# Kernel tuning notes

Measured on AMD Instinct MI355X. Metric: run time of the kernel, lower is better.

The kernel has to match this reference:

```python
import jax, jax.numpy as jnp
import numpy as np

# SamplesLoss(loss='sinkhorn', p=1, blur=0.05): entropic regularization eps = blur**p = 0.05,
# debiased Sinkhorn divergence S(a,b) = OT(a,b) - 0.5*OT(a,a) - 0.5*OT(b,b).
EPS = 0.05
N_ITER = 50
N_POINTS = 32


def _cost(X, Y):
    # p=1 cost: Euclidean distance. X:[B,N,D] Y:[B,M,D] -> [B,N,M]
    d2 = jnp.sum((X[:, :, None, :] - Y[:, None, :, :]) ** 2, axis=-1)
    return jnp.sqrt(d2 + 1e-12)


def _ot(X, Y):
    # log-domain Sinkhorn with uniform weights; returns dual cost <mu,f>+<nu,g> per batch.
    B, N, _ = X.shape
    M = Y.shape[1]
    C = _cost(X, Y)  # [B,N,M]
    log_mu = jnp.full((B, N), -np.log(N), C.dtype)
    log_nu = jnp.full((B, M), -np.log(M), C.dtype)

    def body(carry, _):
        f, g = carry
        f = -EPS * jax.nn.logsumexp((g[:, None, :] - C) / EPS + log_nu[:, None, :], axis=2)
        g = -EPS * jax.nn.logsumexp((f[:, :, None] - C) / EPS + log_mu[:, :, None], axis=1)
        return (f, g), None

    init = (jnp.zeros((B, N), C.dtype), jnp.zeros((B, M), C.dtype))
    (f, g), _ = jax.lax.scan(body, init, None, length=N_ITER)
    return jnp.mean(f, axis=-1) + jnp.mean(g, axis=-1)  # uniform weights => mean


def _sinkhorn_div(X, Y):
    return _ot(X, Y) - 0.5 * _ot(X, X) - 0.5 * _ot(Y, Y)


def _encode(x, W, edge_index):
    # simple 1-layer GCN-style encoder: linear + mean neighbor aggregation + self, ReLU
    h = x @ W  # [n_nodes, emb_dim]
    src, dst = edge_index[0], edge_index[1]
    n = x.shape[0]
    agg = jax.ops.segment_sum(h[src], dst, num_segments=n)
    deg = jax.ops.segment_sum(jnp.ones(src.shape, h.dtype), dst, num_segments=n)
    return jax.nn.relu(h + agg / jnp.maximum(deg, 1.0)[:, None])


def setup_inputs() -> dict:
    key = jax.random.key(0)
    k1, k2, k3, k4, k5 = jax.random.split(key, 5)
    n_nodes, d_feat, emb_dim = 50000, 128, 256
    n_edges, n_pairs = 800000, 8192
    x = jax.random.normal(k1, (n_nodes, d_feat), jnp.float32)
    W = jax.random.normal(k2, (d_feat, emb_dim), jnp.float32) / np.sqrt(d_feat)
    edge_index = jax.random.randint(k3, (2, n_edges), 0, n_nodes, jnp.int64)
    pairs = jax.random.randint(k4, (2, n_pairs), 0, n_nodes, jnp.int64)
    graph_dist = jax.random.uniform(k5, (n_pairs,), jnp.float32, 1.0, 5.0)
    return {"x": x, "W": W, "edge_index": edge_index, "pairs": pairs,
            "graph_dist": graph_dist}


def reference(x, W, edge_index, pairs, graph_dist):
    z = _encode(x, W, edge_index)                       # [n_nodes, emb_dim]
    B = pairs.shape[1]
    Xa = z[pairs[0]].reshape(B, N_POINTS, -1)           # [B, n_points, space_dim]
    Xb = z[pairs[1]].reshape(B, N_POINTS, -1)
    distance = _sinkhorn_div(Xa, Xb)                    # = -score_pairs
    distortion = jnp.abs(distance - graph_dist) / graph_dist
    return jnp.mean(distortion)
```

## Files before the change

kernel.cpp:

```cpp
#include <hip/hip_runtime.h>

#define N_NODES 50000
#define N_EDGES 800000
#define N_PAIRS 8192
#define N_SLOTS (2 * N_PAIRS)
#define CAP     64

#define INV_EPS   20.0f
#define LOG2E_F   1.4426950408889634f
#define LN2_F     0.6931471805599453f
#define LN32_F    3.4657359027997265f
#define EPS_F     0.05f

typedef float f2 __attribute__((ext_vector_type(2)));

__global__ void k_mark(const int* __restrict__ pairs, int* __restrict__ flags) {
    int t = blockIdx.x * 256 + threadIdx.x;
    if (t < N_SLOTS) flags[pairs[t]] = 1;
}

__global__ __launch_bounds__(256) void k_scatter(
        const int* __restrict__ eidx, const int* __restrict__ flags,
        int* __restrict__ cnt, int* __restrict__ bucket) {
    int t = blockIdx.x * 256 + threadIdx.x;
    int dst = eidx[N_EDGES + t];
    if (!flags[dst]) return;
    int pos = atomicAdd(&cnt[dst], 1);
    if (pos < CAP) bucket[dst * CAP + pos] = eidx[t];
}

__global__ __launch_bounds__(256) void k_gemm(
        const int* __restrict__ pairs, const float* __restrict__ x,
        const int* __restrict__ cnt, const int* __restrict__ bucket,
        const float* __restrict__ W, float* __restrict__ Z) {
    __shared__ __align__(16) float Us[16 * 128];
    int sbase = blockIdx.x * 16;
    int t = threadIdx.x;
    int wave = t >> 6, lane = t & 63;

    #pragma unroll
    for (int rr = 0; rr < 4; ++rr) {
        int r = wave * 4 + rr;
        int node = pairs[sbase + r];
        int n = cnt[node];
        int m = (n < CAP) ? n : CAP;
        const int* bk = bucket + node * CAP;
        float ax = 0.0f, ay = 0.0f;
        int k = 0;
        for (; k + 4 <= m; k += 4) {
            int s0 = bk[k], s1 = bk[k + 1], s2 = bk[k + 2], s3 = bk[k + 3];
            float2 v0 = *(const float2*)(x + (size_t)s0 * 128 + lane * 2);
            float2 v1 = *(const float2*)(x + (size_t)s1 * 128 + lane * 2);
            float2 v2 = *(const float2*)(x + (size_t)s2 * 128 + lane * 2);
            float2 v3 = *(const float2*)(x + (size_t)s3 * 128 + lane * 2);
            ax += (v0.x + v1.x) + (v2.x + v3.x);
            ay += (v0.y + v1.y) + (v2.y + v3.y);
        }
        for (; k < m; ++k) {
            int s0 = bk[k];
            float2 v0 = *(const float2*)(x + (size_t)s0 * 128 + lane * 2);
            ax += v0.x;
            ay += v0.y;
        }
        float rdeg = 1.0f / fmaxf((float)n, 1.0f);
        float2 xv = *(const float2*)(x + (size_t)node * 128 + lane * 2);
        float2 o;
        o.x = fmaf(ax, rdeg, xv.x);
        o.y = fmaf(ay, rdeg, xv.y);
        *(float2*)(Us + r * 128 + lane * 2) = o;
    }
    __syncthreads();

    int jq = t & 63;
    int rq = t >> 6;
    float acc[4][4] = {};
    const float4* Wv = (const float4*)W;

    for (int k4 = 0; k4 < 32; ++k4) {
        float4 wv[4];
        #pragma unroll
        for (int i = 0; i < 4; ++i) wv[i] = Wv[(size_t)(k4 * 4 + i) * 64 + jq];
        #pragma unroll
        for (int r = 0; r < 4; ++r) {
            float4 uv = *(const float4*)(Us + (rq * 4 + r) * 128 + k4 * 4);
            float uk0 = uv.x, uk1 = uv.y, uk2 = uv.z, uk3 = uv.w;
            acc[r][0] = fmaf(uk0, wv[0].x, acc[r][0]);
            acc[r][1] = fmaf(uk0, wv[0].y, acc[r][1]);
            acc[r][2] = fmaf(uk0, wv[0].z, acc[r][2]);
            acc[r][3] = fmaf(uk0, wv[0].w, acc[r][3]);
            acc[r][0] = fmaf(uk1, wv[1].x, acc[r][0]);
            acc[r][1] = fmaf(uk1, wv[1].y, acc[r][1]);
            acc[r][2] = fmaf(uk1, wv[1].z, acc[r][2]);
            acc[r][3] = fmaf(uk1, wv[1].w, acc[r][3]);
            acc[r][0] = fmaf(uk2, wv[2].x, acc[r][0]);
            acc[r][1] = fmaf(uk2, wv[2].y, acc[r][1]);
            acc[r][2] = fmaf(uk2, wv[2].z, acc[r][2]);
            acc[r][3] = fmaf(uk2, wv[2].w, acc[r][3]);
            acc[r][0] = fmaf(uk3, wv[3].x, acc[r][0]);
            acc[r][1] = fmaf(uk3, wv[3].y, acc[r][1]);
            acc[r][2] = fmaf(uk3, wv[3].z, acc[r][2]);
            acc[r][3] = fmaf(uk3, wv[3].w, acc[r][3]);
        }
    }

    #pragma unroll
    for (int r = 0; r < 4; ++r) {
        float4 o;
        o.x = fmaxf(acc[r][0], 0.0f);
        o.y = fmaxf(acc[r][1], 0.0f);
        o.z = fmaxf(acc[r][2], 0.0f);
        o.w = fmaxf(acc[r][3], 0.0f);
        *(float4*)(Z + (size_t)(sbase + rq * 4 + r) * 256 + jq * 4) = o;
    }
}

__global__ __launch_bounds__(128) void k_sinkhorn(
        const float* __restrict__ Z, float* __restrict__ dist) {
    __shared__ __align__(16) float smem[2][1280];

    int w = threadIdx.x >> 6;
    int lane = threadIdx.x & 63;
    float* S = &smem[w][0];
    const float CSCALE = -INV_EPS * LOG2E_F;
    const float CBIAS  = -LN32_F * LOG2E_F;

    if (blockIdx.x < 2048) {
        int h = lane >> 5, i = lane & 31;
        int q = (i >> 4) & 1;
        int ip = i ^ 16;
        int P0 = blockIdx.x * 4 + w * 2;

        float* sP   = S;
        float* swv0 = S + 512;
        float* spv0 = S + 576;
        float* swv1 = S + 640;
        float* spv1 = S + 704;

        f2 KA0[8], KB0[8], KA1[8], KB1[8];

        auto build = [&](f2 (&KA)[8], f2 (&KB)[8], int P) {
            int src = h ? (N_PAIRS + P) : P;
            float* sPh = sP + h * 256;
            {
                const float4* zp = (const float4*)(Z + (size_t)src * 256);
                *(float4*)(&sPh[i * 8])     = zp[i * 2];
                *(float4*)(&sPh[i * 8 + 4]) = zp[i * 2 + 1];
            }
            const f2* xp = (const f2*)(&sPh[i * 8]);
            f2 x0 = xp[0], x1 = xp[1], x2 = xp[2], x3 = xp[3];
            const f2* bp = (const f2*)(&sPh[ip * 8]);
            f2 b0 = bp[0], b1 = bp[1], b2 = bp[2], b3 = bp[3];
            #pragma unroll
            for (int t = 0; t < 16; ++t) {
                int j = q * 16 + t;
                const f2* yp = (const f2*)(&sPh[j * 8]);
                f2 y0 = yp[0], y1 = yp[1], y2 = yp[2], y3 = yp[3];
                f2 d, s2;
                d = x0 - y0; s2 = d * d;
                d = x1 - y1; s2 = __builtin_elementwise_fma(d, d, s2);
                d = x2 - y2; s2 = __builtin_elementwise_fma(d, d, s2);
                d = x3 - y3; s2 = __builtin_elementwise_fma(d, d, s2);
                float d2 = s2.x + s2.y + 1e-12f;
                KA[t >> 1][t & 1] = __builtin_amdgcn_exp2f(
                    fmaf(__builtin_amdgcn_sqrtf(d2), CSCALE, CBIAS));
                d = b0 - y0; s2 = d * d;
                d = b1 - y1; s2 = __builtin_elementwise_fma(d, d, s2);
                d = b2 - y2; s2 = __builtin_elementwise_fma(d, d, s2);
                d = b3 - y3; s2 = __builtin_elementwise_fma(d, d, s2);
                float e2 = s2.x + s2.y + 1e-12f;
                KB[t >> 1][t & 1] = __builtin_amdgcn_exp2f(
                    fmaf(__builtin_amdgcn_sqrtf(e2), CSCALE, CBIAS));
            }
        };
        build(KA0, KB0, P0);
        build(KA1, KB1, P0 + 1);

        float pp0 = 0.0f, pp1 = 0.0f, E0 = 1.0f, E1 = 1.0f;
        float w0c = 1.0f, w0p = 1.0f, w1c = 1.0f, w1p = 1.0f;
        swv0[lane] = 1.0f;
        swv1[lane] = 1.0f;

        const int blens[9] = {4, 12, 12, 12, 12, 12, 12, 12, 12};
        #pragma unroll 1
        for (int blk = 0; blk < 9; ++blk) {
            int L = blens[blk];
            #pragma unroll 1
            for (int s = 0; s < L; ++s) {
                const float4* wp0 = (const float4*)(&swv0[h * 32 + q * 16]);
                const float4* wp1 = (const float4*)(&swv1[h * 32 + q * 16]);
                float4 A0 = wp0[0], A1 = wp0[1], A2 = wp0[2], A3 = wp0[3];
                float4 B0 = wp1[0], B1 = wp1[1], B2 = wp1[2], B3 = wp1[3];
                f2 aA0 = KA0[0] * f2{A0.x, A0.y};
                f2 aA1 = KA0[1] * f2{A0.z, A0.w};
                f2 aB0 = KB0[0] * f2{A0.x, A0.y};
                f2 aB1 = KB0[1] * f2{A0.z, A0.w};
                aA0 = __builtin_elementwise_fma(KA0[2], f2{A1.x, A1.y}, aA0);
                aA1 = __builtin_elementwise_fma(KA0[3], f2{A1.z, A1.w}, aA1);
                aB0 = __builtin_elementwise_fma(KB0[2], f2{A1.x, A1.y}, aB0);
                aB1 = __builtin_elementwise_fma(KB0[3], f2{A1.z, A1.w}, aB1);
                aA0 = __builtin_elementwise_fma(KA0[4], f2{A2.x, A2.y}, aA0);
                aA1 = __builtin_elementwise_fma(KA0[5], f2{A2.z, A2.w}, aA1);
                aB0 = __builtin_elementwise_fma(KB0[4], f2{A2.x, A2.y}, aB0);
                aB1 = __builtin_elementwise_fma(KB0[5], f2{A2.z, A2.w}, aB1);
                aA0 = __builtin_elementwise_fma(KA0[6], f2{A3.x, A3.y}, aA0);
                aA1 = __builtin_elementwise_fma(KA0[7], f2{A3.z, A3.w}, aA1);
                aB0 = __builtin_elementwise_fma(KB0[6], f2{A3.x, A3.y}, aB0);
                aB1 = __builtin_elementwise_fma(KB0[7], f2{A3.z, A3.w}, aB1);
                f2 aa0 = aA0 + aA1;
                f2 bb0 = aB0 + aB1;
                float pa0 = aa0.x + aa0.y;
                float pb0 = bb0.x + bb0.y;
                f2 cA0 = KA1[0] * f2{B0.x, B0.y};
                f2 cA1 = KA1[1] * f2{B0.z, B0.w};
                f2 cB0 = KB1[0] * f2{B0.x, B0.y};
                f2 cB1 = KB1[1] * f2{B0.z, B0.w};
                cA0 = __builtin_elementwise_fma(KA1[2], f2{B1.x, B1.y}, cA0);
                cA1 = __builtin_elementwise_fma(KA1[3], f2{B1.z, B1.w}, cA1);
                cB0 = __builtin_elementwise_fma(KB1[2], f2{B1.x, B1.y}, cB0);
                cB1 = __builtin_elementwise_fma(KB1[3], f2{B1.z, B1.w}, cB1);
                cA0 = __builtin_elementwise_fma(KA1[4], f2{B2.x, B2.y}, cA0);
                cA1 = __builtin_elementwise_fma(KA1[5], f2{B2.z, B2.w}, cA1);
                cB0 = __builtin_elementwise_fma(KB1[4], f2{B2.x, B2.y}, cB0);
                cB1 = __builtin_elementwise_fma(KB1[5], f2{B2.z, B2.w}, cB1);
                cA0 = __builtin_elementwise_fma(KA1[6], f2{B3.x, B3.y}, cA0);
                cA1 = __builtin_elementwise_fma(KA1[7], f2{B3.z, B3.w}, cA1);
                cB0 = __builtin_elementwise_fma(KB1[6], f2{B3.x, B3.y}, cB0);
                cB1 = __builtin_elementwise_fma(KB1[7], f2{B3.z, B3.w}, cB1);
                f2 aa1 = cA0 + cA1;
                f2 bb1 = cB0 + cB1;
                float pa1 = aa1.x + aa1.y;
                float pb1 = bb1.x + bb1.y;
                float o0 = __shfl_xor(pb0, 16);
                float o1 = __shfl_xor(pb1, 16);
                w0p = w0c;
                w0c = __builtin_amdgcn_rcpf(pa0 + o0) * E0;
                w1p = w1c;
                w1c = __builtin_amdgcn_rcpf(pa1 + o1) * E1;
                swv0[h * 32 + i] = w0c;
                swv1[h * 32 + i] = w1c;
            }
            if (blk < 8) {
                float d0 = __builtin_amdgcn_logf(w0c);
                float d1 = __builtin_amdgcn_logf(w1c);
                pp0 += d0;
                pp1 += d1;
                spv0[h * 32 + i] = d0;
                spv1[h * 32 + i] = d1;
                {
                    const float4* dv = (const float4*)(&spv0[h * 32 + q * 16]);
                    float4 D0 = dv[0], D1 = dv[1], D2 = dv[2], D3 = dv[3];
                    float ex[16];
                    ex[0]  = __builtin_amdgcn_exp2f(D0.x);
                    ex[1]  = __builtin_amdgcn_exp2f(D0.y);
                    ex[2]  = __builtin_amdgcn_exp2f(D0.z);
                    ex[3]  = __builtin_amdgcn_exp2f(D0.w);
                    ex[4]  = __builtin_amdgcn_exp2f(D1.x);
                    ex[5]  = __builtin_amdgcn_exp2f(D1.y);
                    ex[6]  = __builtin_amdgcn_exp2f(D1.z);
                    ex[7]  = __builtin_amdgcn_exp2f(D1.w);
                    ex[8]  = __builtin_amdgcn_exp2f(D2.x);
                    ex[9]  = __builtin_amdgcn_exp2f(D2.y);
                    ex[10] = __builtin_amdgcn_exp2f(D2.z);
                    ex[11] = __builtin_amdgcn_exp2f(D2.w);
                    ex[12] = __builtin_amdgcn_exp2f(D3.x);
                    ex[13] = __builtin_amdgcn_exp2f(D3.y);
                    ex[14] = __builtin_amdgcn_exp2f(D3.z);
                    ex[15] = __builtin_amdgcn_exp2f(D3.w);
                    #pragma unroll
                    for (int t2 = 0; t2 < 8; ++t2) {
                        f2 ee = f2{ex[2 * t2], ex[2 * t2 + 1]};
                        KA0[t2] *= ee;
                        KB0[t2] *= ee;
                    }
                }
                {
                    const float4* dv = (const float4*)(&spv1[h * 32 + q * 16]);
                    float4 D0 = dv[0], D1 = dv[1], D2 = dv[2], D3 = dv[3];
                    float ex[16];
                    ex[0]  = __builtin_amdgcn_exp2f(D0.x);
                    ex[1]  = __builtin_amdgcn_exp2f(D0.y);
                    ex[2]  = __builtin_amdgcn_exp2f(D0.z);
                    ex[3]  = __builtin_amdgcn_exp2f(D0.w);
                    ex[4]  = __builtin_amdgcn_exp2f(D1.x);
                    ex[5]  = __builtin_amdgcn_exp2f(D1.y);
                    ex[6]  = __builtin_amdgcn_exp2f(D1.z);
                    ex[7]  = __builtin_amdgcn_exp2f(D1.w);
                    ex[8]  = __builtin_amdgcn_exp2f(D2.x);
                    ex[9]  = __builtin_amdgcn_exp2f(D2.y);
                    ex[10] = __builtin_amdgcn_exp2f(D2.z);
                    ex[11] = __builtin_amdgcn_exp2f(D2.w);
                    ex[12] = __builtin_amdgcn_exp2f(D3.x);
                    ex[13] = __builtin_amdgcn_exp2f(D3.y);
                    ex[14] = __builtin_amdgcn_exp2f(D3.z);
                    ex[15] = __builtin_amdgcn_exp2f(D3.w);
                    #pragma unroll
                    for (int t2 = 0; t2 < 8; ++t2) {
                        f2 ee = f2{ex[2 * t2], ex[2 * t2 + 1]};
                        KA1[t2] *= ee;
                        KB1[t2] *= ee;
                    }
                }
                E0 = __builtin_amdgcn_exp2f(-pp0);
                E1 = __builtin_amdgcn_exp2f(-pp1);
                w0c = 1.0f;
                w1c = 1.0f;
                swv0[lane] = 1.0f;
                swv1[lane] = 1.0f;
            }
        }

        float zs0 = 2.0f * pp0 + __builtin_amdgcn_logf(w0p)
                  + __builtin_amdgcn_logf(w0c);
        float zs1 = 2.0f * pp1 + __builtin_amdgcn_logf(w1p)
                  + __builtin_amdgcn_logf(w1c);
        #pragma unroll
        for (int off = 16; off > 0; off >>= 1) {
            zs0 += __shfl_xor(zs0, off);
            zs1 += __shfl_xor(zs1, off);
        }
        if (i == 0) {
            unsafeAtomicAdd(&dist[P0],     -0.5f * (zs0 * (EPS_F * LN2_F / 32.0f)));
            unsafeAtomicAdd(&dist[P0 + 1], -0.5f * (zs1 * (EPS_F * LN2_F / 32.0f)));
        }
    } else {
        int h = lane >> 5, l = lane & 31;
        int p = (blockIdx.x - 2048) * 4 + w * 2 + h;

        float* base = S + h * 640;
        float* sX = base;
        float* sY = base + 256;
        float* sf = base + 512;
        float* sg = base + 544;
        float* su = base + 576;
        float* sv = base + 608;

        {
            const float4* zx = (const float4*)(Z + (size_t)p * 256);
            const float4* zy = (const float4*)(Z + (size_t)(N_PAIRS + p) * 256);
            *(float4*)(&sX[l * 8])     = zx[l * 2];
            *(float4*)(&sX[l * 8 + 4]) = zx[l * 2 + 1];
            *(float4*)(&sY[l * 8])     = zy[l * 2];
            *(float4*)(&sY[l * 8 + 4]) = zy[l * 2 + 1];
        }
        sg[l] = 0.0f;

        f2 Crow[16], Ccol[16];
        {
            const f2* xp = (const f2*)(&sX[l * 8]);
            f2 x0 = xp[0], x1 = xp[1], x2 = xp[2], x3 = xp[3];
            const f2* yp = (const f2*)(&sY[l * 8]);
            f2 y0 = yp[0], y1 = yp[1], y2 = yp[2], y3 = yp[3];
            #pragma unroll
            for (int t = 0; t < 32; ++t) {
                const f2* op = (const f2*)(&sY[t * 8]);
                f2 d, s2;
                d = x0 - op[0]; s2 = d * d;
                d = x1 - op[1]; s2 = __builtin_elementwise_fma(d, d, s2);
                d = x2 - op[2]; s2 = __builtin_elementwise_fma(d, d, s2);
                d = x3 - op[3]; s2 = __builtin_elementwise_fma(d, d, s2);
                float d2 = s2.x + s2.y + 1e-12f;
                Crow[t >> 1][t & 1] = fmaf(__builtin_amdgcn_sqrtf(d2), CSCALE, CBIAS);
                const f2* qp = (const f2*)(&sX[t * 8]);
                d = qp[0] - y0; s2 = d * d;
                d = qp[1] - y1; s2 = __builtin_elementwise_fma(d, d, s2);
                d = qp[2] - y2; s2 = __builtin_elementwise_fma(d, d, s2);
                d = qp[3] - y3; s2 = __builtin_elementwise_fma(d, d, s2);
                float e2 = s2.x + s2.y + 1e-12f;
                Ccol[t >> 1][t & 1] = fmaf(__builtin_amdgcn_sqrtf(e2), CSCALE, CBIAS);
            }
        }

        float ft = 0.0f, gt = 0.0f;

        #pragma unroll 1
        for (int it = 0; it < 2; ++it) {
            {
                const float4* gp = (const float4*)sg;
                float4 G[8];
                #pragma unroll
                for (int r = 0; r < 8; ++r) G[r] = gp[r];
                f2 val[16], m2 = f2{-1e30f, -1e30f};
                #pragma unroll
                for (int r = 0; r < 8; ++r) {
                    val[2 * r]     = f2{G[r].x, G[r].y} + Crow[2 * r];
                    val[2 * r + 1] = f2{G[r].z, G[r].w} + Crow[2 * r + 1];
                    m2 = __builtin_elementwise_max(m2, val[2 * r]);
                    m2 = __builtin_elementwise_max(m2, val[2 * r + 1]);
                }
                float m = fmaxf(m2.x, m2.y);
                f2 mm = f2{m, m};
                float s0 = 0.0f, s1 = 0.0f;
                #pragma unroll
                for (int t2 = 0; t2 < 16; ++t2) {
                    f2 e = val[t2] - mm;
                    s0 += __builtin_amdgcn_exp2f(e.x);
                    s1 += __builtin_amdgcn_exp2f(e.y);
                }
                ft = -(m + __builtin_amdgcn_logf(s0 + s1));
            }
            sf[l] = ft;
            {
                const float4* fp = (const float4*)sf;
                float4 F[8];
                #pragma unroll
                for (int r = 0; r < 8; ++r) F[r] = fp[r];
                f2 val[16], m2 = f2{-1e30f, -1e30f};
                #pragma unroll
                for (int r = 0; r < 8; ++r) {
                    val[2 * r]     = f2{F[r].x, F[r].y} + Ccol[2 * r];
                    val[2 * r + 1] = f2{F[r].z, F[r].w} + Ccol[2 * r + 1];
                    m2 = __builtin_elementwise_max(m2, val[2 * r]);
                    m2 = __builtin_elementwise_max(m2, val[2 * r + 1]);
                }
                float m = fmaxf(m2.x, m2.y);
                f2 mm = f2{m, m};
                float s0 = 0.0f, s1 = 0.0f;
                #pragma unroll
                for (int t2 = 0; t2 < 16; ++t2) {
                    f2 e = val[t2] - mm;
                    s0 += __builtin_amdgcn_exp2f(e.x);
                    s1 += __builtin_amdgcn_exp2f(e.y);
                }
                gt = -(m + __builtin_amdgcn_logf(s0 + s1));
            }
            sg[l] = gt;
        }

        f2 KR[16], KC[16];
        {
            const float4* gp = (const float4*)sg;
            #pragma unroll
            for (int r = 0; r < 8; ++r) {
                float4 G = gp[r];
                f2 a0 = f2{G.x, G.y} + Crow[2 * r] + f2{ft, ft};
                f2 a1 = f2{G.z, G.w} + Crow[2 * r + 1] + f2{ft, ft};
                KR[2 * r].x     = __builtin_amdgcn_exp2f(a0.x);
                KR[2 * r].y     = __builtin_amdgcn_exp2f(a0.y);
                KR[2 * r + 1].x = __builtin_amdgcn_exp2f(a1.x);
                KR[2 * r + 1].y = __builtin_amdgcn_exp2f(a1.y);
            }
            const float4* fp = (const float4*)sf;
            #pragma unroll
            for (int r = 0; r < 8; ++r) {
                float4 F = fp[r];
                f2 a0 = f2{F.x, F.y} + Ccol[2 * r] + f2{gt, gt};
                f2 a1 = f2{F.z, F.w} + Ccol[2 * r + 1] + f2{gt, gt};
                KC[2 * r].x     = __builtin_amdgcn_exp2f(a0.x);
                KC[2 * r].y     = __builtin_amdgcn_exp2f(a0.y);
                KC[2 * r + 1].x = __builtin_amdgcn_exp2f(a1.x);
                KC[2 * r + 1].y = __builtin_amdgcn_exp2f(a1.y);
            }
        }
        sv[l] = 1.0f;
        float ureg = 1.0f, vreg = 1.0f;

        const int blens[5] = {6, 6, 12, 12, 12};
        #pragma unroll 1
        for (int blk = 0; blk < 5; ++blk) {
            int L = blens[blk];
            #pragma unroll 2
            for (int s6 = 0; s6 < L; ++s6) {
                {
                    const float4* vp = (const float4*)sv;
                    f2 acc0, acc1;
                    float4 A = vp[0];
                    acc0 = KR[0] * f2{A.x, A.y};
                    acc1 = KR[1] * f2{A.z, A.w};
                    #pragma unroll
                    for (int r = 1; r < 8; ++r) {
                        float4 B = vp[r];
                        acc0 = __builtin_elementwise_fma(KR[2 * r],     f2{B.x, B.y}, acc0);
                        acc1 = __builtin_elementwise_fma(KR[2 * r + 1], f2{B.z, B.w}, acc1);
                    }
                    f2 a = acc0 + acc1;
                    ureg = __builtin_amdgcn_rcpf(a.x + a.y);
                }
                su[l] = ureg;
                {
                    const float4* up = (const float4*)su;
                    f2 acc0, acc1;
                    float4 A = up[0];
                    acc0 = KC[0] * f2{A.x, A.y};
                    acc1 = KC[1] * f2{A.z, A.w};
                    #pragma unroll
                    for (int r = 1; r < 8; ++r) {
                        float4 B = up[r];
                        acc0 = __builtin_elementwise_fma(KC[2 * r],     f2{B.x, B.y}, acc0);
                        acc1 = __builtin_elementwise_fma(KC[2 * r + 1], f2{B.z, B.w}, acc1);
                    }
                    f2 a = acc0 + acc1;
                    vreg = __builtin_amdgcn_rcpf(a.x + a.y);
                }
                sv[l] = vreg;
            }
            if (blk < 4) {
                float df = __builtin_amdgcn_logf(ureg);
                float dg = __builtin_amdgcn_logf(vreg);
                ft += df;
                gt += dg;
                sf[l] = df;
                sg[l] = dg;
                const float4* dgv = (const float4*)sg;
                #pragma unroll
                for (int r = 0; r < 8; ++r) {
                    float4 D = dgv[r];
                    f2 e0, e1;
                    e0.x = __builtin_amdgcn_exp2f(df + D.x);
                    e0.y = __builtin_amdgcn_exp2f(df + D.y);
                    e1.x = __builtin_amdgcn_exp2f(df + D.z);
                    e1.y = __builtin_amdgcn_exp2f(df + D.w);
                    KR[2 * r]     *= e0;
                    KR[2 * r + 1] *= e1;
                }
                const float4* dfv = (const float4*)sf;
                #pragma unroll
                for (int r = 0; r < 8; ++r) {
                    float4 D = dfv[r];
                    f2 e0, e1;
                    e0.x = __builtin_amdgcn_exp2f(dg + D.x);
                    e0.y = __builtin_amdgcn_exp2f(dg + D.y);
                    e1.x = __builtin_amdgcn_exp2f(dg + D.z);
                    e1.y = __builtin_amdgcn_exp2f(dg + D.w);
                    KC[2 * r]     *= e0;
                    KC[2 * r + 1] *= e1;
                }
                sv[l] = 1.0f;
                ureg = 1.0f;
                vreg = 1.0f;
            }
        }
        ft += __builtin_amdgcn_logf(ureg);
        gt += __builtin_amdgcn_logf(vreg);

        float v = ft + gt;
        #pragma unroll
        for (int off = 16; off > 0; off >>= 1) v += __shfl_xor(v, off);
        if (l == 0) {
            float cost = v * (EPS_F * LN2_F / 32.0f);
            unsafeAtomicAdd(&dist[p], cost);
        }
    }
}

__global__ void k_finalize(const float* __restrict__ dist,
                           const float* __restrict__ gd, float* __restrict__ out) {
    __shared__ float red[256];
    float s = 0.0f;
    for (int i = threadIdx.x; i < N_PAIRS; i += 256) {
        float g = gd[i];
        s += fabsf(dist[i] - g) / g;
    }
    red[threadIdx.x] = s;
    __syncthreads();
    for (int o = 128; o > 0; o >>= 1) {
        if (threadIdx.x < o) red[threadIdx.x] += red[threadIdx.x + o];
        __syncthreads();
    }
    if (threadIdx.x == 0) out[0] = red[0] * (1.0f / N_PAIRS);
}

extern "C" void kernel_launch(void* const* d_in, const int* in_sizes, int n_in,
                              void* d_out, int out_size, void* d_ws, size_t ws_size,
                              hipStream_t stream) {
    const float* x    = (const float*)d_in[0];
    const float* W    = (const float*)d_in[1];
    const int*   eidx = (const int*)d_in[2];
    const int*   pair = (const int*)d_in[3];
    const float* gd   = (const float*)d_in[4];

    char* ws = (char*)d_ws;
    size_t off = 0;
    int*   cnt    = (int*)  (ws + off); off += (size_t)N_NODES * 4;
    int*   flags  = (int*)  (ws + off); off += (size_t)N_NODES * 4;
    float* dist   = (float*)(ws + off); off += (size_t)N_PAIRS * 4;
    size_t zero_bytes = off;
    int*   bucket = (int*)  (ws + off); off += (size_t)N_NODES * CAP * 4;
    float* Z      = (float*)(ws + off); off += (size_t)N_SLOTS * 256 * 4;

    hipMemsetAsync(d_ws, 0, zero_bytes, stream);
    k_mark    <<<(N_SLOTS + 255) / 256, 256, 0, stream>>>(pair, flags);
    k_scatter <<<N_EDGES / 256, 256, 0, stream>>>(eidx, flags, cnt, bucket);
    k_gemm    <<<N_SLOTS / 16, 256, 0, stream>>>(pair, x, cnt, bucket, W, Z);
    k_sinkhorn<<<4096, 128, 0, stream>>>(Z, dist);
    k_finalize<<<1, 256, 0, stream>>>(dist, gd, (float*)d_out);
}
```

Baseline: 242.3 us.

## Drop node-flag marking kernel and fold final reduction into sinkhorn via last-block counter

Removes the k_mark launch and the flag filter in k_scatter, so every edge is now bucketed regardless of whether its destination is used. The separate finalize kernel is replaced by a last-block-done atomic counter inside k_sinkhorn that performs the distortion reduction. This cuts two kernel launches and their gaps. In exchange, the scatter does more atomics and writes for all 800k edges, and the sinkhorn kernel gains an extra sync plus a global atomic per block.

```diff
diff --git a/kernel.cpp b/kernel.cpp
--- a/kernel.cpp
+++ b/kernel.cpp
@@ -1,4 +1,5 @@
 #include <hip/hip_runtime.h>
+#include <hip/hip_runtime_api.h>
 
 #define N_NODES 50000
 #define N_EDGES 800000
@@ -12,19 +13,15 @@
 #define LN32_F    3.4657359027997265f
 #define EPS_F     0.05f
 
+#define SINK_BLOCKS 4096
+
 typedef float f2 __attribute__((ext_vector_type(2)));
 
-__global__ void k_mark(const int* __restrict__ pairs, int* __restrict__ flags) {
-    int t = blockIdx.x * 256 + threadIdx.x;
-    if (t < N_SLOTS) flags[pairs[t]] = 1;
-}
-
 __global__ __launch_bounds__(256) void k_scatter(
-        const int* __restrict__ eidx, const int* __restrict__ flags,
+        const int* __restrict__ eidx,
         int* __restrict__ cnt, int* __restrict__ bucket) {
     int t = blockIdx.x * 256 + threadIdx.x;
     int dst = eidx[N_EDGES + t];
-    if (!flags[dst]) return;
     int pos = atomicAdd(&cnt[dst], 1);
     if (pos < CAP) bucket[dst * CAP + pos] = eidx[t];
 }
@@ -115,8 +112,11 @@
 }
 
 __global__ __launch_bounds__(128) void k_sinkhorn(
-        const float* __restrict__ Z, float* __restrict__ dist) {
+        const float* __restrict__ Z, float* __restrict__ dist,
+        int* __restrict__ done, const float* __restrict__ gd,
+        float* __restrict__ out) {
     __shared__ __align__(16) float smem[2][1280];
+    __shared__ int is_last;
 
     int w = threadIdx.x >> 6;
     int lane = threadIdx.x & 63;
@@ -540,23 +540,32 @@
             unsafeAtomicAdd(&dist[p], cost);
         }
     }
-}
-
-__global__ void k_finalize(const float* __restrict__ dist,
-                           const float* __restrict__ gd, float* __restrict__ out) {
-    __shared__ float red[256];
-    float s = 0.0f;
-    for (int i = threadIdx.x; i < N_PAIRS; i += 256) {
-        float g = gd[i];
-        s += fabsf(dist[i] - g) / g;
+
+    __syncthreads();
+    if (threadIdx.x == 0) {
+        __threadfence();
+        int old = __hip_atomic_fetch_add(done, 1, __ATOMIC_ACQ_REL,
+                                         __HIP_MEMORY_SCOPE_AGENT);
+        is_last = (old == SINK_BLOCKS - 1) ? 1 : 0;
     }
-    red[threadIdx.x] = s;
     __syncthreads();
-    for (int o = 128; o > 0; o >>= 1) {
-        if (threadIdx.x < o) red[threadIdx.x] += red[threadIdx.x + o];
+    if (is_last) {
+        float* red = &smem[0][0];
+        float s = 0.0f;
+        for (int i2 = threadIdx.x; i2 < N_PAIRS; i2 += 128) {
+            float d = __hip_atomic_load(&dist[i2], __ATOMIC_RELAXED,
+                                        __HIP_MEMORY_SCOPE_AGENT);
+            float g = gd[i2];
+            s += fabsf(d - g) / g;
+        }
+        red[threadIdx.x] = s;
         __syncthreads();
+        for (int o = 64; o > 0; o >>= 1) {
+            if (threadIdx.x < o) red[threadIdx.x] += red[threadIdx.x + o];
+            __syncthreads();
+        }
+        if (threadIdx.x == 0) out[0] = red[0] * (1.0f / N_PAIRS);
     }
-    if (threadIdx.x == 0) out[0] = red[0] * (1.0f / N_PAIRS);
 }
 
 extern "C" void kernel_launch(void* const* d_in, const int* in_sizes, int n_in,
@@ -571,16 +580,14 @@
     char* ws = (char*)d_ws;
     size_t off = 0;
     int*   cnt    = (int*)  (ws + off); off += (size_t)N_NODES * 4;
-    int*   flags  = (int*)  (ws + off); off += (size_t)N_NODES * 4;
     float* dist   = (float*)(ws + off); off += (size_t)N_PAIRS * 4;
+    int*   done   = (int*)  (ws + off); off += 128;
     size_t zero_bytes = off;
     int*   bucket = (int*)  (ws + off); off += (size_t)N_NODES * CAP * 4;
     float* Z      = (float*)(ws + off); off += (size_t)N_SLOTS * 256 * 4;
 
     hipMemsetAsync(d_ws, 0, zero_bytes, stream);
-    k_mark    <<<(N_SLOTS + 255) / 256, 256, 0, stream>>>(pair, flags);
-    k_scatter <<<N_EDGES / 256, 256, 0, stream>>>(eidx, flags, cnt, bucket);
+    k_scatter <<<N_EDGES / 256, 256, 0, stream>>>(eidx, cnt, bucket);
     k_gemm    <<<N_SLOTS / 16, 256, 0, stream>>>(pair, x, cnt, bucket, W, Z);
-    k_sinkhorn<<<4096, 128, 0, stream>>>(Z, dist);
-    k_finalize<<<1, 256, 0, stream>>>(dist, gd, (float*)d_out);
+    k_sinkhorn<<<SINK_BLOCKS, 128, 0, stream>>>(Z, dist, done, gd, (float*)d_out);
 }
```

Result: slower. 332.3 us (+37.1%).

## Process two Sinkhorn rows per lane in cross-OT branch, halving its block count

Applied to the files above, without the earlier changes.

In the cross-pair OT branch, each lane now handles two rows and two columns instead of one, so a wavefront covers four pairs instead of two. The cross-branch grid shrinks from 2048 to 1024 blocks and shared memory per block doubles. Each LDS read of the shared g/f/u/v vectors is now reused across two rows, cutting LDS traffic and instruction overhead per unit of work. In exchange, register use per lane roughly doubles (four 32-float cost arrays), which risks lower occupancy or spills.

```diff
diff --git a/kernel.cpp b/kernel.cpp
--- a/kernel.cpp
+++ b/kernel.cpp
@@ -116,7 +116,7 @@
 
 __global__ __launch_bounds__(128) void k_sinkhorn(
         const float* __restrict__ Z, float* __restrict__ dist) {
-    __shared__ __align__(16) float smem[2][1280];
+    __shared__ __align__(16) float smem[2][2560];
 
     int w = threadIdx.x >> 6;
     int lane = threadIdx.x & 63;
@@ -323,10 +323,10 @@
             unsafeAtomicAdd(&dist[P0 + 1], -0.5f * (zs1 * (EPS_F * LN2_F / 32.0f)));
         }
     } else {
-        int h = lane >> 5, l = lane & 31;
-        int p = (blockIdx.x - 2048) * 4 + w * 2 + h;
-
-        float* base = S + h * 640;
+        int g = lane >> 4, r = lane & 15;
+        int p = (blockIdx.x - 2048) * 8 + w * 4 + g;
+
+        float* base = S + g * 640;
         float* sX = base;
         float* sY = base + 256;
         float* sf = base + 512;
@@ -337,40 +337,62 @@
         {
             const float4* zx = (const float4*)(Z + (size_t)p * 256);
             const float4* zy = (const float4*)(Z + (size_t)(N_PAIRS + p) * 256);
-            *(float4*)(&sX[l * 8])     = zx[l * 2];
-            *(float4*)(&sX[l * 8 + 4]) = zx[l * 2 + 1];
-            *(float4*)(&sY[l * 8])     = zy[l * 2];
-            *(float4*)(&sY[l * 8 + 4]) = zy[l * 2 + 1];
-        }
-        sg[l] = 0.0f;
-
-        f2 Crow[16], Ccol[16];
+            float4* x4 = (float4*)sX;
+            float4* y4 = (float4*)sY;
+            #pragma unroll
+            for (int c = 0; c < 4; ++c) {
+                x4[c * 16 + r] = zx[c * 16 + r];
+                y4[c * 16 + r] = zy[c * 16 + r];
+            }
+        }
+        *(f2*)(&sg[2 * r]) = f2{0.0f, 0.0f};
+
+        int i0 = 2 * r, i1 = 2 * r + 1;
+        f2 CrowA[16], CrowB[16], CcolA[16], CcolB[16];
         {
-            const f2* xp = (const f2*)(&sX[l * 8]);
-            f2 x0 = xp[0], x1 = xp[1], x2 = xp[2], x3 = xp[3];
-            const f2* yp = (const f2*)(&sY[l * 8]);
-            f2 y0 = yp[0], y1 = yp[1], y2 = yp[2], y3 = yp[3];
+            const f2* xa = (const f2*)(&sX[i0 * 8]);
+            f2 a0 = xa[0], a1 = xa[1], a2 = xa[2], a3 = xa[3];
+            const f2* xb = (const f2*)(&sX[i1 * 8]);
+            f2 b0 = xb[0], b1 = xb[1], b2 = xb[2], b3 = xb[3];
+            const f2* ya = (const f2*)(&sY[i0 * 8]);
+            f2 c0 = ya[0], c1 = ya[1], c2 = ya[2], c3 = ya[3];
+            const f2* yb = (const f2*)(&sY[i1 * 8]);
+            f2 e0 = yb[0], e1 = yb[1], e2 = yb[2], e3 = yb[3];
             #pragma unroll
             for (int t = 0; t < 32; ++t) {
-                const f2* op = (const f2*)(&sY[t * 8]);
+                const f2* yt = (const f2*)(&sY[t * 8]);
+                f2 y0 = yt[0], y1 = yt[1], y2 = yt[2], y3 = yt[3];
                 f2 d, s2;
-                d = x0 - op[0]; s2 = d * d;
-                d = x1 - op[1]; s2 = __builtin_elementwise_fma(d, d, s2);
-                d = x2 - op[2]; s2 = __builtin_elementwise_fma(d, d, s2);
-                d = x3 - op[3]; s2 = __builtin_elementwise_fma(d, d, s2);
-                float d2 = s2.x + s2.y + 1e-12f;
-                Crow[t >> 1][t & 1] = fmaf(__builtin_amdgcn_sqrtf(d2), CSCALE, CBIAS);
-                const f2* qp = (const f2*)(&sX[t * 8]);
-                d = qp[0] - y0; s2 = d * d;
-                d = qp[1] - y1; s2 = __builtin_elementwise_fma(d, d, s2);
-                d = qp[2] - y2; s2 = __builtin_elementwise_fma(d, d, s2);
-                d = qp[3] - y3; s2 = __builtin_elementwise_fma(d, d, s2);
-                float e2 = s2.x + s2.y + 1e-12f;
-                Ccol[t >> 1][t & 1] = fmaf(__builtin_amdgcn_sqrtf(e2), CSCALE, CBIAS);
-            }
-        }
-
-        float ft = 0.0f, gt = 0.0f;
+                d = a0 - y0; s2 = d * d;
+                d = a1 - y1; s2 = __builtin_elementwise_fma(d, d, s2);
+                d = a2 - y2; s2 = __builtin_elementwise_fma(d, d, s2);
+                d = a3 - y3; s2 = __builtin_elementwise_fma(d, d, s2);
+                float dA = s2.x + s2.y + 1e-12f;
+                CrowA[t >> 1][t & 1] = fmaf(__builtin_amdgcn_sqrtf(dA), CSCALE, CBIAS);
+                d = b0 - y0; s2 = d * d;
+                d = b1 - y1; s2 = __builtin_elementwise_fma(d, d, s2);
+                d = b2 - y2; s2 = __builtin_elementwise_fma(d, d, s2);
+                d = b3 - y3; s2 = __builtin_elementwise_fma(d, d, s2);
+                float dB = s2.x + s2.y + 1e-12f;
+                CrowB[t >> 1][t & 1] = fmaf(__builtin_amdgcn_sqrtf(dB), CSCALE, CBIAS);
+                const f2* xt = (const f2*)(&sX[t * 8]);
+                f2 q0 = xt[0], q1 = xt[1], q2 = xt[2], q3 = xt[3];
+                d = q0 - c0; s2 = d * d;
+                d = q1 - c1; s2 = __builtin_elementwise_fma(d, d, s2);
+                d = q2 - c2; s2 = __builtin_elementwise_fma(d, d, s2);
+                d = q3 - c3; s2 = __builtin_elementwise_fma(d, d, s2);
+                float dC = s2.x + s2.y + 1e-12f;
+                CcolA[t >> 1][t & 1] = fmaf(__builtin_amdgcn_sqrtf(dC), CSCALE, CBIAS);
+                d = q0 - e0; s2 = d * d;
+                d = q1 - e1; s2 = __builtin_elementwise_fma(d, d, s2);
+                d = q2 - e2; s2 = __builtin_elementwise_fma(d, d, s2);
+                d = q3 - e3; s2 = __builtin_elementwise_fma(d, d, s2);
+                float dD = s2.x + s2.y + 1e-12f;
+                CcolB[t >> 1][t & 1] = fmaf(__builtin_amdgcn_sqrtf(dD), CSCALE, CBIAS);
+            }
+        }
+
+        float ft0 = 0.0f, ft1 = 0.0f, gt0 = 0.0f, gt1 = 0.0f;
 
         #pragma unroll 1
         for (int it = 0; it < 2; ++it) {
@@ -378,81 +400,138 @@
                 const float4* gp = (const float4*)sg;
                 float4 G[8];
                 #pragma unroll
-                for (int r = 0; r < 8; ++r) G[r] = gp[r];
-                f2 val[16], m2 = f2{-1e30f, -1e30f};
-                #pragma unroll
-                for (int r = 0; r < 8; ++r) {
-                    val[2 * r]     = f2{G[r].x, G[r].y} + Crow[2 * r];
-                    val[2 * r + 1] = f2{G[r].z, G[r].w} + Crow[2 * r + 1];
-                    m2 = __builtin_elementwise_max(m2, val[2 * r]);
-                    m2 = __builtin_elementwise_max(m2, val[2 * r + 1]);
-                }
-                float m = fmaxf(m2.x, m2.y);
-                f2 mm = f2{m, m};
-                float s0 = 0.0f, s1 = 0.0f;
-                #pragma unroll
-                for (int t2 = 0; t2 < 16; ++t2) {
-                    f2 e = val[t2] - mm;
-                    s0 += __builtin_amdgcn_exp2f(e.x);
-                    s1 += __builtin_amdgcn_exp2f(e.y);
-                }
-                ft = -(m + __builtin_amdgcn_logf(s0 + s1));
-            }
-            sf[l] = ft;
+                for (int r8 = 0; r8 < 8; ++r8) G[r8] = gp[r8];
+                {
+                    f2 val[16], m2 = f2{-1e30f, -1e30f};
+                    #pragma unroll
+                    for (int r8 = 0; r8 < 8; ++r8) {
+                        val[2 * r8]     = f2{G[r8].x, G[r8].y} + CrowA[2 * r8];
+                        val[2 * r8 + 1] = f2{G[r8].z, G[r8].w} + CrowA[2 * r8 + 1];
+                        m2 = __builtin_elementwise_max(m2, val[2 * r8]);
+                        m2 = __builtin_elementwise_max(m2, val[2 * r8 + 1]);
+                    }
+                    float m = fmaxf(m2.x, m2.y);
+                    f2 mm = f2{m, m};
+                    float s0 = 0.0f, s1 = 0.0f;
+                    #pragma unroll
+                    for (int t2 = 0; t2 < 16; ++t2) {
+                        f2 e = val[t2] - mm;
+                        s0 += __builtin_amdgcn_exp2f(e.x);
+                        s1 += __builtin_amdgcn_exp2f(e.y);
+                    }
+                    ft0 = -(m + __builtin_amdgcn_logf(s0 + s1));
+                }
+                {
+                    f2 val[16], m2 = f2{-1e30f, -1e30f};
+                    #pragma unroll
+                    for (int r8 = 0; r8 < 8; ++r8) {
+                        val[2 * r8]     = f2{G[r8].x, G[r8].y} + CrowB[2 * r8];
+                        val[2 * r8 + 1] = f2{G[r8].z, G[r8].w} + CrowB[2 * r8 + 1];
+                        m2 = __builtin_elementwise_max(m2, val[2 * r8]);
+                        m2 = __builtin_elementwise_max(m2, val[2 * r8 + 1]);
+                    }
+                    float m = fmaxf(m2.x, m2.y);
+                    f2 mm = f2{m, m};
+                    float s0 = 0.0f, s1 = 0.0f;
+                    #pragma unroll
+                    for (int t2 = 0; t2 < 16; ++t2) {
+                        f2 e = val[t2] - mm;
+                        s0 += __builtin_amdgcn_exp2f(e.x);
+                        s1 += __builtin_amdgcn_exp2f(e.y);
+                    }
+                    ft1 = -(m + __builtin_amdgcn_logf(s0 + s1));
+                }
+            }
+            *(f2*)(&sf[2 * r]) = f2{ft0, ft1};
             {
                 const float4* fp = (const float4*)sf;
                 float4 F[8];
                 #pragma unroll
-                for (int r = 0; r < 8; ++r) F[r] = fp[r];
-                f2 val[16], m2 = f2{-1e30f, -1e30f};
-                #pragma unroll
-                for (int r = 0; r < 8; ++r) {
-                    val[2 * r]     = f2{F[r].x, F[r].y} + Ccol[2 * r];
-                    val[2 * r + 1] = f2{F[r].z, F[r].w} + Ccol[2 * r + 1];
-                    m2 = __builtin_elementwise_max(m2, val[2 * r]);
-                    m2 = __builtin_elementwise_max(m2, val[2 * r + 1]);
-                }
-                float m = fmaxf(m2.x, m2.y);
-                f2 mm = f2{m, m};
-                float s0 = 0.0f, s1 = 0.0f;
-                #pragma unroll
-                for (int t2 = 0; t2 < 16; ++t2) {
-                    f2 e = val[t2] - mm;
-                    s0 += __builtin_amdgcn_exp2f(e.x);
-                    s1 += __builtin_amdgcn_exp2f(e.y);
-                }
-                gt = -(m + __builtin_amdgcn_logf(s0 + s1));
-            }
-            sg[l] = gt;
-        }
-
-        f2 KR[16], KC[16];
+                for (int r8 = 0; r8 < 8; ++r8) F[r8] = fp[r8];
+                {
+                    f2 val[16], m2 = f2{-1e30f, -1e30f};
+                    #pragma unroll
+                    for (int r8 = 0; r8 < 8; ++r8) {
+                        val[2 * r8]     = f2{F[r8].x, F[r8].y} + CcolA[2 * r8];
+                        val[2 * r8 + 1] = f2{F[r8].z, F[r8].w} + CcolA[2 * r8 + 1];
+                        m2 = __builtin_elementwise_max(m2, val[2 * r8]);
+                        m2 = __builtin_elementwise_max(m2, val[2 * r8 + 1]);
+                    }
+                    float m = fmaxf(m2.x, m2.y);
+                    f2 mm = f2{m, m};
+                    float s0 = 0.0f, s1 = 0.0f;
+                    #pragma unroll
+                    for (int t2 = 0; t2 < 16; ++t2) {
+                        f2 e = val[t2] - mm;
+                        s0 += __builtin_amdgcn_exp2f(e.x);
+                        s1 += __builtin_amdgcn_exp2f(e.y);
+                    }
+                    gt0 = -(m + __builtin_amdgcn_logf(s0 + s1));
+                }
+                {
+                    f2 val[16], m2 = f2{-1e30f, -1e30f};
+                    #pragma unroll
+                    for (int r8 = 0; r8 < 8; ++r8) {
+                        val[2 * r8]     = f2{F[r8].x, F[r8].y} + CcolB[2 * r8];
+                        val[2 * r8 + 1] = f2{F[r8].z, F[r8].w} + CcolB[2 * r8 + 1];
+                        m2 = __builtin_elementwise_max(m2, val[2 * r8]);
+                        m2 = __builtin_elementwise_max(m2, val[2 * r8 + 1]);
+                    }
+                    float m = fmaxf(m2.x, m2.y);
+                    f2 mm = f2{m, m};
+                    float s0 = 0.0f, s1 = 0.0f;
+                    #pragma unroll
+                    for (int t2 = 0; t2 < 16; ++t2) {
+                        f2 e = val[t2] - mm;
+                        s0 += __builtin_amdgcn_exp2f(e.x);
+                        s1 += __builtin_amdgcn_exp2f(e.y);
+                    }
+                    gt1 = -(m + __builtin_amdgcn_logf(s0 + s1));
+                }
+            }
+            *(f2*)(&sg[2 * r]) = f2{gt0, gt1};
+        }
+
         {
             const float4* gp = (const float4*)sg;
             #pragma unroll
-            for (int r = 0; r < 8; ++r) {
-                float4 G = gp[r];
-                f2 a0 = f2{G.x, G.y} + Crow[2 * r] + f2{ft, ft};
-                f2 a1 = f2{G.z, G.w} + Crow[2 * r + 1] + f2{ft, ft};
-                KR[2 * r].x     = __builtin_amdgcn_exp2f(a0.x);
-                KR[2 * r].y     = __builtin_amdgcn_exp2f(a0.y);
-                KR[2 * r + 1].x = __builtin_amdgcn_exp2f(a1.x);
-                KR[2 * r + 1].y = __builtin_amdgcn_exp2f(a1.y);
+            for (int r8 = 0; r8 < 8; ++r8) {
+                float4 G = gp[r8];
+                f2 t0, t1;
+                t0 = CrowA[2 * r8]     + f2{G.x, G.y} + f2{ft0, ft0};
+                t1 = CrowA[2 * r8 + 1] + f2{G.z, G.w} + f2{ft0, ft0};
+                CrowA[2 * r8].x     = __builtin_amdgcn_exp2f(t0.x);
+                CrowA[2 * r8].y     = __builtin_amdgcn_exp2f(t0.y);
+                CrowA[2 * r8 + 1].x = __builtin_amdgcn_exp2f(t1.x);
+                CrowA[2 * r8 + 1].y = __builtin_amdgcn_exp2f(t1.y);
+                t0 = CrowB[2 * r8]     + f2{G.x, G.y} + f2{ft1, ft1};
+                t1 = CrowB[2 * r8 + 1] + f2{G.z, G.w} + f2{ft1, ft1};
+                CrowB[2 * r8].x     = __builtin_amdgcn_exp2f(t0.x);
+                CrowB[2 * r8].y     = __builtin_amdgcn_exp2f(t0.y);
+                CrowB[2 * r8 + 1].x = __builtin_amdgcn_exp2f(t1.x);
+                CrowB[2 * r8 + 1].y = __builtin_amdgcn_exp2f(t1.y);
             }
             const float4* fp = (const float4*)sf;
             #pragma unroll
-            for (int r = 0; r < 8; ++r) {
-                float4 F = fp[r];
-                f2 a0 = f2{F.x, F.y} + Ccol[2 * r] + f2{gt, gt};
-                f2 a1 = f2{F.z, F.w} + Ccol[2 * r + 1] + f2{gt, gt};
-                KC[2 * r].x     = __builtin_amdgcn_exp2f(a0.x);
-                KC[2 * r].y     = __builtin_amdgcn_exp2f(a0.y);
-                KC[2 * r + 1].x = __builtin_amdgcn_exp2f(a1.x);
-                KC[2 * r + 1].y = __builtin_amdgcn_exp2f(a1.y);
-            }
-        }
-        sv[l] = 1.0f;
-        float ureg = 1.0f, vreg = 1.0f;
+            for (int r8 = 0; r8 < 8; ++r8) {
+                float4 F = fp[r8];
+                f2 t0, t1;
+                t0 = CcolA[2 * r8]     + f2{F.x, F.y} + f2{gt0, gt0};
+                t1 = CcolA[2 * r8 + 1] + f2{F.z, F.w} + f2{gt0, gt0};
+                CcolA[2 * r8].x     = __builtin_amdgcn_exp2f(t0.x);
+                CcolA[2 * r8].y     = __builtin_amdgcn_exp2f(t0.y);
+                CcolA[2 * r8 + 1].x = __builtin_amdgcn_exp2f(t1.x);
+                CcolA[2 * r8 + 1].y = __builtin_amdgcn_exp2f(t1.y);
+                t0 = CcolB[2 * r8]     + f2{F.x, F.y} + f2{gt1, gt1};
+                t1 = CcolB[2 * r8 + 1] + f2{F.z, F.w} + f2{gt1, gt1};
+                CcolB[2 * r8].x     = __builtin_amdgcn_exp2f(t0.x);
+                CcolB[2 * r8].y     = __builtin_amdgcn_exp2f(t0.y);
+                CcolB[2 * r8 + 1].x = __builtin_amdgcn_exp2f(t1.x);
+                CcolB[2 * r8 + 1].y = __builtin_amdgcn_exp2f(t1.y);
+            }
+        }
+        *(f2*)(&sv[2 * r]) = f2{1.0f, 1.0f};
+        float u0 = 1.0f, u1 = 1.0f, v0 = 1.0f, v1 = 1.0f;
 
         const int blens[5] = {6, 6, 12, 12, 12};
         #pragma unroll 1
@@ -462,81 +541,107 @@
             for (int s6 = 0; s6 < L; ++s6) {
                 {
                     const float4* vp = (const float4*)sv;
-                    f2 acc0, acc1;
+                    f2 aA0, aA1, aB0, aB1;
                     float4 A = vp[0];
-                    acc0 = KR[0] * f2{A.x, A.y};
-                    acc1 = KR[1] * f2{A.z, A.w};
-                    #pragma unroll
-                    for (int r = 1; r < 8; ++r) {
-                        float4 B = vp[r];
-                        acc0 = __builtin_elementwise_fma(KR[2 * r],     f2{B.x, B.y}, acc0);
-                        acc1 = __builtin_elementwise_fma(KR[2 * r + 1], f2{B.z, B.w}, acc1);
-                    }
-                    f2 a = acc0 + acc1;
-                    ureg = __builtin_amdgcn_rcpf(a.x + a.y);
-                }
-                su[l] = ureg;
+                    aA0 = CrowA[0] * f2{A.x, A.y};
+                    aA1 = CrowA[1] * f2{A.z, A.w};
+                    aB0 = CrowB[0] * f2{A.x, A.y};
+                    aB1 = CrowB[1] * f2{A.z, A.w};
+                    #pragma unroll
+                    for (int rr = 1; rr < 8; ++rr) {
+                        float4 B = vp[rr];
+                        aA0 = __builtin_elementwise_fma(CrowA[2 * rr],     f2{B.x, B.y}, aA0);
+                        aA1 = __builtin_elementwise_fma(CrowA[2 * rr + 1], f2{B.z, B.w}, aA1);
+                        aB0 = __builtin_elementwise_fma(CrowB[2 * rr],     f2{B.x, B.y}, aB0);
+                        aB1 = __builtin_elementwise_fma(CrowB[2 * rr + 1], f2{B.z, B.w}, aB1);
+                    }
+                    f2 sa = aA0 + aA1;
+                    f2 sb = aB0 + aB1;
+                    u0 = __builtin_amdgcn_rcpf(sa.x + sa.y);
+                    u1 = __builtin_amdgcn_rcpf(sb.x + sb.y);
+                }
+                *(f2*)(&su[2 * r]) = f2{u0, u1};
                 {
                     const float4* up = (const float4*)su;
-                    f2 acc0, acc1;
+                    f2 aA0, aA1, aB0, aB1;
                     float4 A = up[0];
-                    acc0 = KC[0] * f2{A.x, A.y};
-                    acc1 = KC[1] * f2{A.z, A.w};
-                    #pragma unroll
-                    for (int r = 1; r < 8; ++r) {
-                        float4 B = up[r];
-                        acc0 = __builtin_elementwise_fma(KC[2 * r],     f2{B.x, B.y}, acc0);
-                        acc1 = __builtin_elementwise_fma(KC[2 * r + 1], f2{B.z, B.w}, acc1);
-                    }
-                    f2 a = acc0 + acc1;
-                    vreg = __builtin_amdgcn_rcpf(a.x + a.y);
-                }
-                sv[l] = vreg;
+                    aA0 = CcolA[0] * f2{A.x, A.y};
+                    aA1 = CcolA[1] * f2{A.z, A.w};
+                    aB0 = CcolB[0] * f2{A.x, A.y};
+                    aB1 = CcolB[1] * f2{A.z, A.w};
+                    #pragma unroll
+                    for (int rr = 1; rr < 8; ++rr) {
+                        float4 B = up[rr];
+                        aA0 = __builtin_elementwise_fma(CcolA[2 * rr],     f2{B.x, B.y}, aA0);
+                        aA1 = __builtin_elementwise_fma(CcolA[2 * rr + 1], f2{B.z, B.w}, aA1);
+                        aB0 = __builtin_elementwise_fma(CcolB[2 * rr],     f2{B.x, B.y}, aB0);
+                        aB1 = __builtin_elementwise_fma(CcolB[2 * rr + 1], f2{B.z, B.w}, aB1);
+                    }
+                    f2 sa = aA0 + aA1;
+                    f2 sb = aB0 + aB1;
+                    v0 = __builtin_amdgcn_rcpf(sa.x + sa.y);
+                    v1 = __builtin_amdgcn_rcpf(sb.x + sb.y);
+                }
+                *(f2*)(&sv[2 * r]) = f2{v0, v1};
             }
             if (blk < 4) {
-                float df = __builtin_amdgcn_logf(ureg);
-                float dg = __builtin_amdgcn_logf(vreg);
-                ft += df;
-                gt += dg;
-                sf[l] = df;
-                sg[l] = dg;
+                float df0 = __builtin_amdgcn_logf(u0);
+                float df1 = __builtin_amdgcn_logf(u1);
+                float dg0 = __builtin_amdgcn_logf(v0);
+                float dg1 = __builtin_amdgcn_logf(v1);
+                ft0 += df0; ft1 += df1; gt0 += dg0; gt1 += dg1;
+                *(f2*)(&sf[2 * r]) = f2{df0, df1};
+                *(f2*)(&sg[2 * r]) = f2{dg0, dg1};
                 const float4* dgv = (const float4*)sg;
                 #pragma unroll
-                for (int r = 0; r < 8; ++r) {
-                    float4 D = dgv[r];
-                    f2 e0, e1;
-                    e0.x = __builtin_amdgcn_exp2f(df + D.x);
-                    e0.y = __builtin_amdgcn_exp2f(df + D.y);
-                    e1.x = __builtin_amdgcn_exp2f(df + D.z);
-                    e1.y = __builtin_amdgcn_exp2f(df + D.w);
-                    KR[2 * r]     *= e0;
-                    KR[2 * r + 1] *= e1;
+                for (int r8 = 0; r8 < 8; ++r8) {
+                    float4 D = dgv[r8];
+                    f2 eA0, eA1, eB0, eB1;
+                    eA0.x = __builtin_amdgcn_exp2f(df0 + D.x);
+                    eA0.y = __builtin_amdgcn_exp2f(df0 + D.y);
+                    eA1.x = __builtin_amdgcn_exp2f(df0 + D.z);
+                    eA1.y = __builtin_amdgcn_exp2f(df0 + D.w);
+                    eB0.x = __builtin_amdgcn_exp2f(df1 + D.x);
+                    eB0.y = __builtin_amdgcn_exp2f(df1 + D.y);
+                    eB1.x = __builtin_amdgcn_exp2f(df1 + D.z);
+                    eB1.y = __builtin_amdgcn_exp2f(df1 + D.w);
+                    CrowA[2 * r8]     *= eA0;
+                    CrowA[2 * r8 + 1] *= eA1;
+                    CrowB[2 * r8]     *= eB0;
+                    CrowB[2 * r8 + 1] *= eB1;
                 }
                 const float4* dfv = (const float4*)sf;
                 #pragma unroll
-                for (int r = 0; r < 8; ++r) {
-                    float4 D = dfv[r];
-                    f2 e0, e1;
-                    e0.x = __builtin_amdgcn_exp2f(dg + D.x);
-                    e0.y = __builtin_amdgcn_exp2f(dg + D.y);
-                    e1.x = __builtin_amdgcn_exp2f(dg + D.z);
-                    e1.y = __builtin_amdgcn_exp2f(dg + D.w);
-                    KC[2 * r]     *= e0;
-                    KC[2 * r + 1] *= e1;
-                }
-                sv[l] = 1.0f;
-                ureg = 1.0f;
-                vreg = 1.0f;
-            }
-        }
-        ft += __builtin_amdgcn_logf(ureg);
-        gt += __builtin_amdgcn_logf(vreg);
-
-        float v = ft + gt;
+                for (int r8 = 0; r8 < 8; ++r8) {
+                    float4 D = dfv[r8];
+                    f2 eA0, eA1, eB0, eB1;
+                    eA0.x = __builtin_amdgcn_exp2f(dg0 + D.x);
+                    eA0.y = __builtin_amdgcn_exp2f(dg0 + D.y);
+                    eA1.x = __builtin_amdgcn_exp2f(dg0 + D.z);
+                    eA1.y = __builtin_amdgcn_exp2f(dg0 + D.w);
+                    eB0.x = __builtin_amdgcn_exp2f(dg1 + D.x);
+                    eB0.y = __builtin_amdgcn_exp2f(dg1 + D.y);
+                    eB1.x = __builtin_amdgcn_exp2f(dg1 + D.z);
+                    eB1.y = __builtin_amdgcn_exp2f(dg1 + D.w);
+                    CcolA[2 * r8]     *= eA0;
+                    CcolA[2 * r8 + 1] *= eA1;
+                    CcolB[2 * r8]     *= eB0;
+                    CcolB[2 * r8 + 1] *= eB1;
+                }
+                *(f2*)(&sv[2 * r]) = f2{1.0f, 1.0f};
+                u0 = 1.0f; u1 = 1.0f; v0 = 1.0f; v1 = 1.0f;
+            }
+        }
+        ft0 += __builtin_amdgcn_logf(u0);
+        ft1 += __builtin_amdgcn_logf(u1);
+        gt0 += __builtin_amdgcn_logf(v0);
+        gt1 += __builtin_amdgcn_logf(v1);
+
+        float vs = (ft0 + ft1) + (gt0 + gt1);
         #pragma unroll
-        for (int off = 16; off > 0; off >>= 1) v += __shfl_xor(v, off);
-        if (l == 0) {
-            float cost = v * (EPS_F * LN2_F / 32.0f);
+        for (int off = 8; off > 0; off >>= 1) vs += __shfl_xor(vs, off);
+        if (r == 0) {
+            float cost = vs * (EPS_F * LN2_F / 32.0f);
             unsafeAtomicAdd(&dist[p], cost);
         }
     }
@@ -581,6 +686,6 @@
     k_mark    <<<(N_SLOTS + 255) / 256, 256, 0, stream>>>(pair, flags);
     k_scatter <<<N_EDGES / 256, 256, 0, stream>>>(eidx, flags, cnt, bucket);
     k_gemm    <<<N_SLOTS / 16, 256, 0, stream>>>(pair, x, cnt, bucket, W, Z);
-    k_sinkhorn<<<4096, 128, 0, stream>>>(Z, dist);
+    k_sinkhorn<<<3072, 128, 0, stream>>>(Z, dist);
     k_finalize<<<1, 256, 0, stream>>>(dist, gd, (float*)d_out);
 }
```

Result: slower. 249.6 us (+3.0%).
